# Kernel optimization log

Hardware: AMD Instinct MI355X
Metric: run time of the kernel (lower is better)

## Reference

```python
import jax, jax.numpy as jnp
import numpy as np

B, S, D = 4, 2048, 2048
H, KVH = 16, 8
HD = D // H          # 128
N_REP = H // KVH     # 2


def _rope(t, cos, sin):
    # t: [B,S,h,HD]; cos/sin: [S, HD//2]
    tr = t.reshape(*t.shape[:-1], HD // 2, 2)
    t0, t1 = tr[..., 0], tr[..., 1]
    c = cos[None, :, None, :]
    s = sin[None, :, None, :]
    o0 = t0 * c - t1 * s
    o1 = t0 * s + t1 * c
    return jnp.stack([o0, o1], axis=-1).reshape(t.shape)


def setup_inputs() -> dict:
    key = jax.random.key(0)
    ks = jax.random.split(key, 7)
    x = jax.random.normal(ks[0], (B, S, D), dtype=jnp.float32)
    wq = jax.random.normal(ks[1], (D, H * HD), dtype=jnp.float32) * 0.02
    wk = jax.random.normal(ks[2], (D, KVH * HD), dtype=jnp.float32) * 0.02
    wv = jax.random.normal(ks[3], (D, KVH * HD), dtype=jnp.float32) * 0.02
    wo = jax.random.normal(ks[4], (H * HD, D), dtype=jnp.float32) * 0.02
    # rotary angles as in precompute_pos_cis: theta=1e6-style base 10000
    freqs = 1.0 / (10000.0 ** (jnp.arange(0, HD, 2, dtype=jnp.float32) / HD))
    ang = jnp.outer(jnp.arange(S, dtype=jnp.float32), freqs)  # [S, HD//2]
    return {"x": x, "wq": wq, "wk": wk, "wv": wv, "wo": wo,
            "pos_cos": jnp.cos(ang), "pos_sin": jnp.sin(ang)}


def reference(x, wq, wk, wv, wo, pos_cos, pos_sin):
    q = (x @ wq).reshape(B, S, H, HD)
    k = (x @ wk).reshape(B, S, KVH, HD)
    v = (x @ wv).reshape(B, S, KVH, HD)
    q = _rope(q, pos_cos, pos_sin)
    k = _rope(k, pos_cos, pos_sin)
    # GQA repeat_kv: [B,S,KVH,HD] -> [B,S,H,HD]
    k = jnp.repeat(k, N_REP, axis=2)
    v = jnp.repeat(v, N_REP, axis=2)
    scale = 1.0 / jnp.sqrt(jnp.float32(HD))
    scores = jnp.einsum('bqhd,bkhd->bhqk', q, k) * scale
    causal = jnp.tril(jnp.ones((S, S), dtype=bool))
    scores = jnp.where(causal[None, None], scores, jnp.float32(-jnp.inf))
    attn = jax.nn.softmax(scores, axis=-1)
    out = jnp.einsum('bhqk,bkhd->bqhd', attn, v).reshape(B, S, H * HD)
    return out @ wo
```

## Files before the change

### kernel.cpp

```cpp
#include <hip/hip_runtime.h>
#include <stdint.h>

#define SEQ   2048
#define DIM   2048
#define NH    16
#define NKVH  8
#define HDIM  128
#define MTOT  8192
#define LOG2E 1.44269504088896340736f

typedef short bf16x8 __attribute__((ext_vector_type(8)));
typedef float f32x4  __attribute__((ext_vector_type(4)));
typedef unsigned short us4 __attribute__((ext_vector_type(4)));

#define MFMA(a, b, c) __builtin_amdgcn_mfma_f32_16x16x32_bf16((a), (b), (c), 0, 0, 0)

__device__ inline unsigned short f2bf(float f) {
    unsigned u = __builtin_bit_cast(unsigned, f);
    u = (u + 0x7FFFu + ((u >> 16) & 1u)) >> 16;
    return (unsigned short)u;
}

__device__ inline void stage16(const void* g, void* l) {
    __builtin_amdgcn_global_load_lds(
        (const __attribute__((address_space(1))) void*)g,
        (__attribute__((address_space(3))) void*)l,
        16, 0, 0);
}

__global__ void conv_x(const float* __restrict__ x, unsigned short* __restrict__ xb) {
    long i = ((long)blockIdx.x * 256 + threadIdx.x) * 4;
    float4 v = *(const float4*)(x + i);
    us4 o = { f2bf(v.x), f2bf(v.y), f2bf(v.z), f2bf(v.w) };
    *(us4*)(xb + i) = o;
}

__global__ void transpose_w(const float* __restrict__ in, unsigned short* __restrict__ out,
                            int N, int row_off) {
    __shared__ float t[32][33];
    int tx = threadIdx.x, ty = threadIdx.y;
    int n0 = blockIdx.x * 32, k0 = blockIdx.y * 32;
    for (int i = 0; i < 4; i++)
        t[ty + i * 8][tx] = in[(long)(k0 + ty + i * 8) * N + n0 + tx];
    __syncthreads();
    for (int i = 0; i < 4; i++)
        out[(long)(row_off + n0 + ty + i * 8) * 2048 + k0 + tx] = f2bf(t[tx][ty + i * 8]);
}

__global__ void transpose_v(const unsigned short* __restrict__ v, unsigned short* __restrict__ vt) {
    __shared__ unsigned short t[32][33];
    int tx = threadIdx.x, ty = threadIdx.y;
    int d0 = blockIdx.x * 32, s0 = blockIdx.y * 32, bk = blockIdx.z;
    const unsigned short* vin = v + (long)bk * SEQ * HDIM;
    unsigned short* vo = vt + (long)bk * HDIM * SEQ;
    for (int i = 0; i < 4; i++)
        t[ty + i * 8][tx] = vin[(long)(s0 + ty + i * 8) * HDIM + d0 + tx];
    __syncthreads();
    for (int i = 0; i < 4; i++)
        vo[(long)(d0 + ty + i * 8) * SEQ + s0 + tx] = t[tx][ty + i * 8];
}


#define STAGEH(p_, op_, h_, t_) do {                                              \
    unsigned short* d_ = sh + (p_) * 32768 + (op_) * 16384 + (h_) * 8192 + tid * 8; \
    const unsigned short* s_ = ((op_) ? bg : ag) + (long)((h_) * 128) * K + (t_) * 64; \
    stage16(s_, d_); stage16(s_ + 64 * K, d_ + 4096); } while (0)

#define BARRIER() asm volatile("s_barrier" ::: "memory")
#define WAITLGKM() asm volatile("s_waitcnt lgkmcnt(0)" ::: "memory")

__launch_bounds__(512, 2)
__global__ void qkv_gemm(const unsigned short* __restrict__ xb,
                         const unsigned short* __restrict__ wt,
                         const float* __restrict__ pcos, const float* __restrict__ psin,
                         unsigned short* __restrict__ qb, unsigned short* __restrict__ kbuf,
                         unsigned short* __restrict__ vbuf) {
    constexpr int K  = DIM;
    constexpr int NT = K / 64;
    __shared__ __align__(16) unsigned short sh[65536];
    const int tid = threadIdx.x;
    const int m0 = blockIdx.y * 256;
    const int n0 = blockIdx.x * 256;
    const int w = tid >> 6, lane = tid & 63, qq = lane >> 4, ln = lane & 15;
    const int wm = w >> 2, wn = w & 3;

    f32x4 acc[8][4] = {};

    const int rowq = tid >> 3;
    const int cswz = ((tid & 7) ^ (rowq & 7)) * 8;
    const unsigned short* ag = xb + (long)(m0 + rowq) * K + cswz;
    const unsigned short* bg = wt + (long)(n0 + rowq) * K + cswz;

    const int aoff = wm * 8192 + ln * 64;
    const int boff = 16384 + (wn >> 1) * 8192 + ((wn & 1) * 64 + ln) * 64;
    const int swz0 = ((0 + qq) ^ (ln & 7)) * 8;
    const int swz1 = ((4 + qq) ^ (ln & 7)) * 8;

    STAGEH(0, 1, 0, 0); STAGEH(0, 1, 1, 0); STAGEH(0, 0, 0, 0); STAGEH(0, 0, 1, 0);
    STAGEH(1, 1, 0, 1); STAGEH(1, 0, 0, 1); STAGEH(1, 0, 1, 1);

    #pragma unroll 1
    for (int t = 0; t < NT; t++) {
        const int p = t & 1, pn = p ^ 1;
        if (t >= NT - 1) asm volatile("s_waitcnt vmcnt(0)" ::: "memory");
        else             asm volatile("s_waitcnt vmcnt(6)" ::: "memory");
        BARRIER();

        const unsigned short* Ab = sh + p * 32768;
        bf16x8 af[8][2], bf_[4][2];

        #pragma unroll
        for (int fc = 0; fc < 4; fc++) {
            bf_[fc][0] = *(const bf16x8*)&Ab[boff + fc * 1024 + swz0];
            bf_[fc][1] = *(const bf16x8*)&Ab[boff + fc * 1024 + swz1];
        }
        #pragma unroll
        for (int fr = 0; fr < 4; fr++) {
            af[fr][0] = *(const bf16x8*)&Ab[aoff + fr * 1024 + swz0];
            af[fr][1] = *(const bf16x8*)&Ab[aoff + fr * 1024 + swz1];
        }
        if (t + 1 < NT) STAGEH(pn, 1, 1, t + 1);
        BARRIER();
        WAITLGKM();
        __builtin_amdgcn_s_setprio(1);
        #pragma unroll
        for (int fr = 0; fr < 4; fr++)
            #pragma unroll
            for (int fc = 0; fc < 2; fc++) {
                acc[fr][fc] = MFMA(bf_[fc][0], af[fr][0], acc[fr][fc]);
                acc[fr][fc] = MFMA(bf_[fc][1], af[fr][1], acc[fr][fc]);
            }
        __builtin_amdgcn_s_setprio(0);
        BARRIER();

        #pragma unroll
        for (int fr = 4; fr < 8; fr++) {
            af[fr][0] = *(const bf16x8*)&Ab[aoff + fr * 1024 + swz0];
            af[fr][1] = *(const bf16x8*)&Ab[aoff + fr * 1024 + swz1];
        }
        if (t + 2 < NT) STAGEH(p, 1, 0, t + 2);
        BARRIER();
        WAITLGKM();
        __builtin_amdgcn_s_setprio(1);
        #pragma unroll
        for (int fr = 0; fr < 4; fr++)
            #pragma unroll
            for (int fc = 2; fc < 4; fc++) {
                acc[fr][fc] = MFMA(bf_[fc][0], af[fr][0], acc[fr][fc]);
                acc[fr][fc] = MFMA(bf_[fc][1], af[fr][1], acc[fr][fc]);
            }
        __builtin_amdgcn_s_setprio(0);
        BARRIER();

        if (t + 2 < NT) STAGEH(p, 0, 0, t + 2);
        BARRIER();
        __builtin_amdgcn_s_setprio(1);
        #pragma unroll
        for (int fr = 4; fr < 8; fr++)
            #pragma unroll
            for (int fc = 0; fc < 2; fc++) {
                acc[fr][fc] = MFMA(bf_[fc][0], af[fr][0], acc[fr][fc]);
                acc[fr][fc] = MFMA(bf_[fc][1], af[fr][1], acc[fr][fc]);
            }
        __builtin_amdgcn_s_setprio(0);
        BARRIER();

        if (t + 2 < NT) STAGEH(p, 0, 1, t + 2);
        BARRIER();
        __builtin_amdgcn_s_setprio(1);
        #pragma unroll
        for (int fr = 4; fr < 8; fr++)
            #pragma unroll
            for (int fc = 2; fc < 4; fc++) {
                acc[fr][fc] = MFMA(bf_[fc][0], af[fr][0], acc[fr][fc]);
                acc[fr][fc] = MFMA(bf_[fc][1], af[fr][1], acc[fr][fc]);
            }
        __builtin_amdgcn_s_setprio(0);
        BARRIER();
    }

    const bool isv = (n0 >= 3072);
    for (int fr = 0; fr < 8; fr++) {
        int m = m0 + wm * 128 + fr * 16 + ln;
        int b_ = m >> 11, s = m & (SEQ - 1);
        const float* crow = pcos + s * 64;
        const float* srow = psin + s * 64;
        for (int fc = 0; fc < 4; fc++) {
            int n = n0 + wn * 64 + fc * 16 + qq * 4;
            int d = n & (HDIM - 1);
            f32x4 v = acc[fr][fc];
            float o0, o1, o2, o3;
            if (!isv) {
                int i = d >> 1;
                float2 cc = *(const float2*)(crow + i);
                float2 ss = *(const float2*)(srow + i);
                o0 = v[0] * cc.x - v[1] * ss.x;
                o1 = v[0] * ss.x + v[1] * cc.x;
                o2 = v[2] * cc.y - v[3] * ss.y;
                o3 = v[2] * ss.y + v[3] * cc.y;
            } else {
                o0 = v[0]; o1 = v[1]; o2 = v[2]; o3 = v[3];
            }
            us4 pu = { f2bf(o0), f2bf(o1), f2bf(o2), f2bf(o3) };
            if (n < 2048) {
                int hh = n >> 7;
                *(us4*)&qb[((long)(b_ * NH + hh) * SEQ + s) * HDIM + d] = pu;
            } else if (n < 3072) {
                int kvh = (n - 2048) >> 7;
                *(us4*)&kbuf[((long)(b_ * NKVH + kvh) * SEQ + s) * HDIM + d] = pu;
            } else {
                int kvh = (n - 3072) >> 7;
                *(us4*)&vbuf[((long)(b_ * NKVH + kvh) * SEQ + s) * HDIM + d] = pu;
            }
        }
    }
}

__launch_bounds__(256, 2)
__global__ void flash(const unsigned short* __restrict__ qb,
                      const unsigned short* __restrict__ kb,
                      const unsigned short* __restrict__ vtb,
                      unsigned short* __restrict__ aout) {
    __shared__ __align__(16) unsigned short KV[32768];
    const int tid = threadIdx.x;
    const int w = tid >> 6, lane = tid & 63, qq = lane >> 4, ln = lane & 15;
    unsigned short* Pseg = KV + w * 4096;

    int f = blockIdx.x + (blockIdx.y << 3) + (blockIdx.z << 7);
    int xcd = f & 7, j = f >> 3;
    int bkv = xcd + 8 * (j & 3);
    int b = bkv >> 3, kv = bkv & 7;
    int rem = j >> 2;
    int h = kv * 2 + (rem & 1);
    int qpair = rem >> 1;

    const unsigned short* qbase = qb + (long)(b * NH + h) * SEQ * HDIM;
    const unsigned short* kbase = kb + (long)(b * NKVH + kv) * SEQ * HDIM;
    const unsigned short* vbase = vtb + (long)(b * NKVH + kv) * HDIM * SEQ;
    const float SCL2 = 0.088388347648318447f * LOG2E;

    const int srow = tid >> 4;
    const int sswz = (tid & 15) ^ srow;

    for (int phase = 0; phase < 2; phase++) {
        const int qt = (phase == 0) ? qpair : 15 - qpair;
        const int q0 = qt * 128 + w * 32;

        bf16x8 qf[2][4];
        for (int nt = 0; nt < 2; nt++)
            for (int ks = 0; ks < 4; ks++)
                qf[nt][ks] = *(const bf16x8*)&qbase[(long)(q0 + nt * 16 + ln) * HDIM + ks * 32 + qq * 8];

        float m[2] = { -3e38f, -3e38f }, l[2] = { 0.f, 0.f };
        f32x4 oacc[8][2] = {};

        #pragma unroll 1
        for (int kt = 0; kt <= qt; kt++) {
            const int k0 = kt * 128;

            __syncthreads();
            char* kl = (char*)KV;
            #pragma unroll
            for (int r = 0; r < 8; r++) {
                int key = r * 16 + srow;
                stage16(kbase + (long)(k0 + key) * HDIM + sswz * 8, kl + r * 4096 + tid * 16);
            }
            #pragma unroll
            for (int r = 0; r < 8; r++) {
                int hd = r * 16 + srow;
                stage16(vbase + (long)hd * SEQ + k0 + sswz * 8, kl + 32768 + r * 4096 + tid * 16);
            }
            __syncthreads();

            f32x4 sacc[8][2] = {};
            #pragma unroll
            for (int mt = 0; mt < 8; mt++) {
                const unsigned short* kr = &KV[(mt * 16 + ln) * 128];
                bf16x8 kf0 = *(const bf16x8*)&kr[((0 + qq) ^ ln) * 8];
                bf16x8 kf1 = *(const bf16x8*)&kr[((4 + qq) ^ ln) * 8];
                bf16x8 kf2 = *(const bf16x8*)&kr[((8 + qq) ^ ln) * 8];
                bf16x8 kf3 = *(const bf16x8*)&kr[((12 + qq) ^ ln) * 8];
                sacc[mt][0] = MFMA(kf0, qf[0][0], sacc[mt][0]);
                sacc[mt][1] = MFMA(kf0, qf[1][0], sacc[mt][1]);
                sacc[mt][0] = MFMA(kf1, qf[0][1], sacc[mt][0]);
                sacc[mt][1] = MFMA(kf1, qf[1][1], sacc[mt][1]);
                sacc[mt][0] = MFMA(kf2, qf[0][2], sacc[mt][0]);
                sacc[mt][1] = MFMA(kf2, qf[1][2], sacc[mt][1]);
                sacc[mt][0] = MFMA(kf3, qf[0][3], sacc[mt][0]);
                sacc[mt][1] = MFMA(kf3, qf[1][3], sacc[mt][1]);
            }

            __syncthreads();

            const bool diag = (kt == qt);
            #pragma unroll
            for (int nt = 0; nt < 2; nt++) {
                const int q = q0 + nt * 16 + ln;
                float mx = m[nt];
                #pragma unroll
                for (int mt = 0; mt < 8; mt++)
                    #pragma unroll
                    for (int r = 0; r < 4; r++) {
                        float v = sacc[mt][nt][r];
                        if (diag && (k0 + mt * 16 + qq * 4 + r > q)) v = -3e38f;
                        sacc[mt][nt][r] = v;
                        mx = fmaxf(mx, v);
                    }
                mx = fmaxf(mx, __shfl_xor(mx, 16));
                mx = fmaxf(mx, __shfl_xor(mx, 32));
                float alpha = exp2f((m[nt] - mx) * SCL2);
                m[nt] = mx;
                float rs = 0.f;
                #pragma unroll
                for (int mt = 0; mt < 8; mt++) {
                    float p0 = exp2f((sacc[mt][nt][0] - mx) * SCL2);
                    float p1 = exp2f((sacc[mt][nt][1] - mx) * SCL2);
                    float p2 = exp2f((sacc[mt][nt][2] - mx) * SCL2);
                    float p3 = exp2f((sacc[mt][nt][3] - mx) * SCL2);
                    rs += (p0 + p1) + (p2 + p3);
                    us4 pu = { f2bf(p0), f2bf(p1), f2bf(p2), f2bf(p3) };
                    *(us4*)&Pseg[(nt * 16 + ln) * 128 + ((mt * 2 + (qq >> 1)) ^ ln) * 8 + (qq & 1) * 4] = pu;
                }
                rs += __shfl_xor(rs, 16);
                rs += __shfl_xor(rs, 32);
                l[nt] = l[nt] * alpha + rs;
                #pragma unroll
                for (int mt = 0; mt < 8; mt++)
                    #pragma unroll
                    for (int r = 0; r < 4; r++)
                        oacc[mt][nt][r] *= alpha;
            }

            bf16x8 pf[4][2];
            #pragma unroll
            for (int ks = 0; ks < 4; ks++)
                #pragma unroll
                for (int nt = 0; nt < 2; nt++)
                    pf[ks][nt] = *(const bf16x8*)&Pseg[(nt * 16 + ln) * 128 + ((ks * 4 + qq) ^ ln) * 8];
            #pragma unroll
            for (int mt = 0; mt < 8; mt++) {
                const unsigned short* vr = &KV[16384 + (mt * 16 + ln) * 128];
                bf16x8 vf0 = *(const bf16x8*)&vr[((0 + qq) ^ ln) * 8];
                bf16x8 vf1 = *(const bf16x8*)&vr[((4 + qq) ^ ln) * 8];
                bf16x8 vf2 = *(const bf16x8*)&vr[((8 + qq) ^ ln) * 8];
                bf16x8 vf3 = *(const bf16x8*)&vr[((12 + qq) ^ ln) * 8];
                oacc[mt][0] = MFMA(vf0, pf[0][0], oacc[mt][0]);
                oacc[mt][1] = MFMA(vf0, pf[0][1], oacc[mt][1]);
                oacc[mt][0] = MFMA(vf1, pf[1][0], oacc[mt][0]);
                oacc[mt][1] = MFMA(vf1, pf[1][1], oacc[mt][1]);
                oacc[mt][0] = MFMA(vf2, pf[2][0], oacc[mt][0]);
                oacc[mt][1] = MFMA(vf2, pf[2][1], oacc[mt][1]);
                oacc[mt][0] = MFMA(vf3, pf[3][0], oacc[mt][0]);
                oacc[mt][1] = MFMA(vf3, pf[3][1], oacc[mt][1]);
            }
        }

        #pragma unroll
        for (int nt = 0; nt < 2; nt++) {
            const int q = q0 + nt * 16 + ln;
            float inv = 1.f / l[nt];
            unsigned short* ao = aout + ((long)b * SEQ + q) * DIM + h * HDIM;
            #pragma unroll
            for (int mt = 0; mt < 8; mt++) {
                us4 o = { f2bf(oacc[mt][nt][0] * inv), f2bf(oacc[mt][nt][1] * inv),
                          f2bf(oacc[mt][nt][2] * inv), f2bf(oacc[mt][nt][3] * inv) };
                *(us4*)&ao[mt * 16 + qq * 4] = o;
            }
        }
    }
}

__launch_bounds__(512, 2)
__global__ void out_gemm(const unsigned short* __restrict__ ab,
                         const unsigned short* __restrict__ wt,
                         float* __restrict__ out) {
    constexpr int K  = DIM;
    constexpr int NT = K / 64;
    __shared__ __align__(16) unsigned short sh[65536];
    const int tid = threadIdx.x;
    const int m0 = blockIdx.y * 256;
    const int n0 = blockIdx.x * 256;
    const int w = tid >> 6, lane = tid & 63, qq = lane >> 4, ln = lane & 15;
    const int wm = w >> 2, wn = w & 3;

    f32x4 acc[8][4] = {};

    const int rowq = tid >> 3;
    const int cswz = ((tid & 7) ^ (rowq & 7)) * 8;
    const unsigned short* ag = ab + (long)(m0 + rowq) * K + cswz;
    const unsigned short* bg = wt + (long)(n0 + rowq) * K + cswz;

    const int aoff = wm * 8192 + ln * 64;
    const int boff = 16384 + (wn >> 1) * 8192 + ((wn & 1) * 64 + ln) * 64;
    const int swz0 = ((0 + qq) ^ (ln & 7)) * 8;
    const int swz1 = ((4 + qq) ^ (ln & 7)) * 8;

    STAGEH(0, 1, 0, 0); STAGEH(0, 1, 1, 0); STAGEH(0, 0, 0, 0); STAGEH(0, 0, 1, 0);
    STAGEH(1, 1, 0, 1); STAGEH(1, 0, 0, 1); STAGEH(1, 0, 1, 1);

    #pragma unroll 1
    for (int t = 0; t < NT; t++) {
        const int p = t & 1, pn = p ^ 1;
        if (t >= NT - 1) asm volatile("s_waitcnt vmcnt(0)" ::: "memory");
        else             asm volatile("s_waitcnt vmcnt(6)" ::: "memory");
        BARRIER();

        const unsigned short* Ab = sh + p * 32768;
        bf16x8 af[8][2], bf_[4][2];

        #pragma unroll
        for (int fc = 0; fc < 4; fc++) {
            bf_[fc][0] = *(const bf16x8*)&Ab[boff + fc * 1024 + swz0];
            bf_[fc][1] = *(const bf16x8*)&Ab[boff + fc * 1024 + swz1];
        }
        #pragma unroll
        for (int fr = 0; fr < 4; fr++) {
            af[fr][0] = *(const bf16x8*)&Ab[aoff + fr * 1024 + swz0];
            af[fr][1] = *(const bf16x8*)&Ab[aoff + fr * 1024 + swz1];
        }
        if (t + 1 < NT) STAGEH(pn, 1, 1, t + 1);
        BARRIER();
        WAITLGKM();
        __builtin_amdgcn_s_setprio(1);
        #pragma unroll
        for (int fr = 0; fr < 4; fr++)
            #pragma unroll
            for (int fc = 0; fc < 2; fc++) {
                acc[fr][fc] = MFMA(af[fr][0], bf_[fc][0], acc[fr][fc]);
                acc[fr][fc] = MFMA(af[fr][1], bf_[fc][1], acc[fr][fc]);
            }
        __builtin_amdgcn_s_setprio(0);
        BARRIER();

        #pragma unroll
        for (int fr = 4; fr < 8; fr++) {
            af[fr][0] = *(const bf16x8*)&Ab[aoff + fr * 1024 + swz0];
            af[fr][1] = *(const bf16x8*)&Ab[aoff + fr * 1024 + swz1];
        }
        if (t + 2 < NT) STAGEH(p, 1, 0, t + 2);
        BARRIER();
        WAITLGKM();
        __builtin_amdgcn_s_setprio(1);
        #pragma unroll
        for (int fr = 0; fr < 4; fr++)
            #pragma unroll
            for (int fc = 2; fc < 4; fc++) {
                acc[fr][fc] = MFMA(af[fr][0], bf_[fc][0], acc[fr][fc]);
                acc[fr][fc] = MFMA(af[fr][1], bf_[fc][1], acc[fr][fc]);
            }
        __builtin_amdgcn_s_setprio(0);
        BARRIER();

        if (t + 2 < NT) STAGEH(p, 0, 0, t + 2);
        BARRIER();
        __builtin_amdgcn_s_setprio(1);
        #pragma unroll
        for (int fr = 4; fr < 8; fr++)
            #pragma unroll
            for (int fc = 0; fc < 2; fc++) {
                acc[fr][fc] = MFMA(af[fr][0], bf_[fc][0], acc[fr][fc]);
                acc[fr][fc] = MFMA(af[fr][1], bf_[fc][1], acc[fr][fc]);
            }
        __builtin_amdgcn_s_setprio(0);
        BARRIER();

        if (t + 2 < NT) STAGEH(p, 0, 1, t + 2);
        BARRIER();
        __builtin_amdgcn_s_setprio(1);
        #pragma unroll
        for (int fr = 4; fr < 8; fr++)
            #pragma unroll
            for (int fc = 2; fc < 4; fc++) {
                acc[fr][fc] = MFMA(af[fr][0], bf_[fc][0], acc[fr][fc]);
                acc[fr][fc] = MFMA(af[fr][1], bf_[fc][1], acc[fr][fc]);
            }
        __builtin_amdgcn_s_setprio(0);
        BARRIER();
    }

    for (int fr = 0; fr < 8; fr++)
        for (int fc = 0; fc < 4; fc++) {
            int n = n0 + wn * 64 + fc * 16 + ln;
            for (int r = 0; r < 4; r++) {
                int m = m0 + wm * 128 + fr * 16 + qq * 4 + r;
                out[(long)m * DIM + n] = acc[fr][fc][r];
            }
        }
}

extern "C" void kernel_launch(void* const* d_in, const int* in_sizes, int n_in,
                              void* d_out, int out_size, void* d_ws, size_t ws_size,
                              hipStream_t stream) {
    const float* x    = (const float*)d_in[0];
    const float* wq   = (const float*)d_in[1];
    const float* wk   = (const float*)d_in[2];
    const float* wv   = (const float*)d_in[3];
    const float* wo   = (const float*)d_in[4];
    const float* pcos = (const float*)d_in[5];
    const float* psin = (const float*)d_in[6];
    float* out = (float*)d_out;

    char* ws = (char*)d_ws;
    unsigned short* xb    = (unsigned short*)(ws);
    unsigned short* wqkvt = (unsigned short*)(ws + 33554432L);
    unsigned short* wot   = (unsigned short*)(ws + 50331648L);
    unsigned short* qbuf  = (unsigned short*)(ws + 58720256L);
    unsigned short* kbuf  = (unsigned short*)(ws + 92274688L);
    unsigned short* vbuf  = (unsigned short*)(ws + 109051904L);
    unsigned short* vtb   = (unsigned short*)(ws + 125829120L);
    unsigned short* aout  = (unsigned short*)(ws + 142606336L);

    conv_x<<<16384, 256, 0, stream>>>(x, xb);
    transpose_w<<<dim3(64, 64), dim3(32, 8), 0, stream>>>(wq, wqkvt, 2048, 0);
    transpose_w<<<dim3(32, 64), dim3(32, 8), 0, stream>>>(wk, wqkvt, 1024, 2048);
    transpose_w<<<dim3(32, 64), dim3(32, 8), 0, stream>>>(wv, wqkvt, 1024, 3072);
    transpose_w<<<dim3(64, 64), dim3(32, 8), 0, stream>>>(wo, wot, 2048, 0);

    qkv_gemm<<<dim3(16, 32), 512, 0, stream>>>(xb, wqkvt, pcos, psin, qbuf, kbuf, vbuf);
    transpose_v<<<dim3(4, 64, 32), dim3(32, 8), 0, stream>>>(vbuf, vtb);
    flash<<<dim3(8, 16, 4), 256, 0, stream>>>(qbuf, kbuf, vtb, aout);
    out_gemm<<<dim3(8, 32), 512, 0, stream>>>(aout, wot, out);
}
```

Measured before the change: 512.1 us.

## Replace pipelined 256x256 QKV GEMM with simple 128x128 tile; raise MFMA priority in flash

The QKV projection GEMM drops its double-buffered, barrier-interleaved 256x256 tile schedule for a plain single-buffered 128x128 tile loop with 256 threads. The grid grows fourfold. Separately, the flash attention kernel wraps its QK and PV MFMA loops in s_setprio to favour matrix issue. The simpler GEMM loses overlap between global loads and compute and reuses less data per tile, so more memory traffic is likely. The extra blocks may help occupancy.

Result: slower. 544.7 us (+6.4%).

```diff
diff --git a/kernel.cpp b/kernel.cpp
--- a/kernel.cpp
+++ b/kernel.cpp
@@ -60,135 +60,64 @@
         vo[(long)(d0 + ty + i * 8) * SEQ + s0 + tx] = t[tx][ty + i * 8];
 }
 
-
-#define STAGEH(p_, op_, h_, t_) do {                                              \
-    unsigned short* d_ = sh + (p_) * 32768 + (op_) * 16384 + (h_) * 8192 + tid * 8; \
-    const unsigned short* s_ = ((op_) ? bg : ag) + (long)((h_) * 128) * K + (t_) * 64; \
-    stage16(s_, d_); stage16(s_ + 64 * K, d_ + 4096); } while (0)
-
-#define BARRIER() asm volatile("s_barrier" ::: "memory")
-#define WAITLGKM() asm volatile("s_waitcnt lgkmcnt(0)" ::: "memory")
-
-__launch_bounds__(512, 2)
+__launch_bounds__(256, 2)
 __global__ void qkv_gemm(const unsigned short* __restrict__ xb,
                          const unsigned short* __restrict__ wt,
                          const float* __restrict__ pcos, const float* __restrict__ psin,
                          unsigned short* __restrict__ qb, unsigned short* __restrict__ kbuf,
                          unsigned short* __restrict__ vbuf) {
-    constexpr int K  = DIM;
-    constexpr int NT = K / 64;
-    __shared__ __align__(16) unsigned short sh[65536];
+    constexpr int K = DIM;
+    __shared__ __align__(16) unsigned short As[128 * 64];
+    __shared__ __align__(16) unsigned short Bs[128 * 64];
     const int tid = threadIdx.x;
-    const int m0 = blockIdx.y * 256;
-    const int n0 = blockIdx.x * 256;
+    const int m0 = blockIdx.y * 128;
+    const int n0 = blockIdx.x * 128;
     const int w = tid >> 6, lane = tid & 63, qq = lane >> 4, ln = lane & 15;
-    const int wm = w >> 2, wn = w & 3;
-
-    f32x4 acc[8][4] = {};
-
-    const int rowq = tid >> 3;
-    const int cswz = ((tid & 7) ^ (rowq & 7)) * 8;
-    const unsigned short* ag = xb + (long)(m0 + rowq) * K + cswz;
-    const unsigned short* bg = wt + (long)(n0 + rowq) * K + cswz;
-
-    const int aoff = wm * 8192 + ln * 64;
-    const int boff = 16384 + (wn >> 1) * 8192 + ((wn & 1) * 64 + ln) * 64;
-    const int swz0 = ((0 + qq) ^ (ln & 7)) * 8;
-    const int swz1 = ((4 + qq) ^ (ln & 7)) * 8;
-
-    STAGEH(0, 1, 0, 0); STAGEH(0, 1, 1, 0); STAGEH(0, 0, 0, 0); STAGEH(0, 0, 1, 0);
-    STAGEH(1, 1, 0, 1); STAGEH(1, 0, 0, 1); STAGEH(1, 0, 1, 1);
-
-    #pragma unroll 1
-    for (int t = 0; t < NT; t++) {
-        const int p = t & 1, pn = p ^ 1;
-        if (t >= NT - 1) asm volatile("s_waitcnt vmcnt(0)" ::: "memory");
-        else             asm volatile("s_waitcnt vmcnt(6)" ::: "memory");
-        BARRIER();
-
-        const unsigned short* Ab = sh + p * 32768;
-        bf16x8 af[8][2], bf_[4][2];
-
-        #pragma unroll
-        for (int fc = 0; fc < 4; fc++) {
-            bf_[fc][0] = *(const bf16x8*)&Ab[boff + fc * 1024 + swz0];
-            bf_[fc][1] = *(const bf16x8*)&Ab[boff + fc * 1024 + swz1];
-        }
-        #pragma unroll
-        for (int fr = 0; fr < 4; fr++) {
-            af[fr][0] = *(const bf16x8*)&Ab[aoff + fr * 1024 + swz0];
-            af[fr][1] = *(const bf16x8*)&Ab[aoff + fr * 1024 + swz1];
-        }
-        if (t + 1 < NT) STAGEH(pn, 1, 1, t + 1);
-        BARRIER();
-        WAITLGKM();
-        __builtin_amdgcn_s_setprio(1);
-        #pragma unroll
-        for (int fr = 0; fr < 4; fr++)
-            #pragma unroll
-            for (int fc = 0; fc < 2; fc++) {
-                acc[fr][fc] = MFMA(bf_[fc][0], af[fr][0], acc[fr][fc]);
-                acc[fr][fc] = MFMA(bf_[fc][1], af[fr][1], acc[fr][fc]);
-            }
-        __builtin_amdgcn_s_setprio(0);
-        BARRIER();
-
-        #pragma unroll
-        for (int fr = 4; fr < 8; fr++) {
-            af[fr][0] = *(const bf16x8*)&Ab[aoff + fr * 1024 + swz0];
-            af[fr][1] = *(const bf16x8*)&Ab[aoff + fr * 1024 + swz1];
-        }
-        if (t + 2 < NT) STAGEH(p, 1, 0, t + 2);
-        BARRIER();
-        WAITLGKM();
-        __builtin_amdgcn_s_setprio(1);
-        #pragma unroll
-        for (int fr = 0; fr < 4; fr++)
-            #pragma unroll
-            for (int fc = 2; fc < 4; fc++) {
-                acc[fr][fc] = MFMA(bf_[fc][0], af[fr][0], acc[fr][fc]);
-                acc[fr][fc] = MFMA(bf_[fc][1], af[fr][1], acc[fr][fc]);
-            }
-        __builtin_amdgcn_s_setprio(0);
-        BARRIER();
-
-        if (t + 2 < NT) STAGEH(p, 0, 0, t + 2);
-        BARRIER();
-        __builtin_amdgcn_s_setprio(1);
-        #pragma unroll
-        for (int fr = 4; fr < 8; fr++)
-            #pragma unroll
-            for (int fc = 0; fc < 2; fc++) {
-                acc[fr][fc] = MFMA(bf_[fc][0], af[fr][0], acc[fr][fc]);
-                acc[fr][fc] = MFMA(bf_[fc][1], af[fr][1], acc[fr][fc]);
-            }
-        __builtin_amdgcn_s_setprio(0);
-        BARRIER();
-
-        if (t + 2 < NT) STAGEH(p, 0, 1, t + 2);
-        BARRIER();
-        __builtin_amdgcn_s_setprio(1);
-        #pragma unroll
-        for (int fr = 4; fr < 8; fr++)
-            #pragma unroll
-            for (int fc = 2; fc < 4; fc++) {
-                acc[fr][fc] = MFMA(bf_[fc][0], af[fr][0], acc[fr][fc]);
-                acc[fr][fc] = MFMA(bf_[fc][1], af[fr][1], acc[fr][fc]);
-            }
-        __builtin_amdgcn_s_setprio(0);
-        BARRIER();
+    const int wm = w >> 1, wn = w & 1;
+
+    f32x4 acc[4][4] = {};
+
+    const int arow = tid >> 3;
+    const int aswz = ((tid & 7) ^ (arow & 7)) * 8;
+    const unsigned short* ag = xb + (long)(m0 + arow) * K + aswz;
+    const unsigned short* bg = wt + (long)(n0 + arow) * K + aswz;
+    unsigned short* al = As + tid * 8;
+    unsigned short* bl = Bs + tid * 8;
+
+    for (int kk = 0; kk < K; kk += 64) {
+        __syncthreads();
+        stage16(ag + kk,          al);
+        stage16(ag + kk + 32 * K, al + 2048);
+        stage16(ag + kk + 64 * K, al + 4096);
+        stage16(ag + kk + 96 * K, al + 6144);
+        stage16(bg + kk,          bl);
+        stage16(bg + kk + 32 * K, bl + 2048);
+        stage16(bg + kk + 64 * K, bl + 4096);
+        stage16(bg + kk + 96 * K, bl + 6144);
+        __syncthreads();
+        bf16x8 a[2][4], b[2][4];
+        for (int ks = 0; ks < 2; ks++) {
+            for (int mt = 0; mt < 4; mt++)
+                a[ks][mt] = *(const bf16x8*)&As[(wm * 64 + mt * 16 + ln) * 64 + (((ks * 4 + qq) ^ (ln & 7)) * 8)];
+            for (int nt = 0; nt < 4; nt++)
+                b[ks][nt] = *(const bf16x8*)&Bs[(wn * 64 + nt * 16 + ln) * 64 + (((ks * 4 + qq) ^ (ln & 7)) * 8)];
+        }
+        for (int ks = 0; ks < 2; ks++)
+            for (int mt = 0; mt < 4; mt++)
+                for (int nt = 0; nt < 4; nt++)
+                    acc[mt][nt] = MFMA(b[ks][nt], a[ks][mt], acc[mt][nt]);
     }
 
     const bool isv = (n0 >= 3072);
-    for (int fr = 0; fr < 8; fr++) {
-        int m = m0 + wm * 128 + fr * 16 + ln;
+    for (int mt = 0; mt < 4; mt++) {
+        int m = m0 + wm * 64 + mt * 16 + ln;
         int b_ = m >> 11, s = m & (SEQ - 1);
         const float* crow = pcos + s * 64;
         const float* srow = psin + s * 64;
-        for (int fc = 0; fc < 4; fc++) {
-            int n = n0 + wn * 64 + fc * 16 + qq * 4;
+        for (int nt = 0; nt < 4; nt++) {
+            int n = n0 + wn * 64 + nt * 16 + qq * 4;
             int d = n & (HDIM - 1);
-            f32x4 v = acc[fr][fc];
+            f32x4 v = acc[mt][nt];
             float o0, o1, o2, o3;
             if (!isv) {
                 int i = d >> 1;
@@ -273,6 +202,7 @@
             __syncthreads();
 
             f32x4 sacc[8][2] = {};
+            __builtin_amdgcn_s_setprio(1);
             #pragma unroll
             for (int mt = 0; mt < 8; mt++) {
                 const unsigned short* kr = &KV[(mt * 16 + ln) * 128];
@@ -289,6 +219,7 @@
                 sacc[mt][0] = MFMA(kf3, qf[0][3], sacc[mt][0]);
                 sacc[mt][1] = MFMA(kf3, qf[1][3], sacc[mt][1]);
             }
+            __builtin_amdgcn_s_setprio(0);
 
             __syncthreads();
 
@@ -337,6 +268,7 @@
                 #pragma unroll
                 for (int nt = 0; nt < 2; nt++)
                     pf[ks][nt] = *(const bf16x8*)&Pseg[(nt * 16 + ln) * 128 + ((ks * 4 + qq) ^ ln) * 8];
+            __builtin_amdgcn_s_setprio(1);
             #pragma unroll
             for (int mt = 0; mt < 8; mt++) {
                 const unsigned short* vr = &KV[16384 + (mt * 16 + ln) * 128];
@@ -353,6 +285,7 @@
                 oacc[mt][0] = MFMA(vf3, pf[3][0], oacc[mt][0]);
                 oacc[mt][1] = MFMA(vf3, pf[3][1], oacc[mt][1]);
             }
+            __builtin_amdgcn_s_setprio(0);
         }
 
         #pragma unroll
@@ -369,6 +302,15 @@
         }
     }
 }
+
+
+#define STAGEH(p_, op_, h_, t_) do {                                              \
+    unsigned short* d_ = sh + (p_) * 32768 + (op_) * 16384 + (h_) * 8192 + tid * 8; \
+    const unsigned short* s_ = ((op_) ? bg : ag) + (long)((h_) * 128) * K + (t_) * 64; \
+    stage16(s_, d_); stage16(s_ + 64 * K, d_ + 4096); } while (0)
+
+#define BARRIER() asm volatile("s_barrier" ::: "memory")
+#define WAITLGKM() asm volatile("s_waitcnt lgkmcnt(0)" ::: "memory")
 
 __launch_bounds__(512, 2)
 __global__ void out_gemm(const unsigned short* __restrict__ ab,
@@ -516,7 +458,7 @@
     transpose_w<<<dim3(32, 64), dim3(32, 8), 0, stream>>>(wv, wqkvt, 1024, 3072);
     transpose_w<<<dim3(64, 64), dim3(32, 8), 0, stream>>>(wo, wot, 2048, 0);
 
-    qkv_gemm<<<dim3(16, 32), 512, 0, stream>>>(xb, wqkvt, pcos, psin, qbuf, kbuf, vbuf);
+    qkv_gemm<<<dim3(32, 64), 256, 0, stream>>>(xb, wqkvt, pcos, psin, qbuf, kbuf, vbuf);
     transpose_v<<<dim3(4, 64, 32), dim3(32, 8), 0, stream>>>(vbuf, vtb);
     flash<<<dim3(8, 16, 4), 256, 0, stream>>>(qbuf, kbuf, vtb, aout);
     out_gemm<<<dim3(8, 32), 512, 0, stream>>>(aout, wot, out);
```

## Simplify QKV GEMM pipeline, split attention waits, add lazy softmax rescaling

Applied to the files above, without the earlier changes.

The QKV GEMM drops its fine-grained half-tile staging, which had many barriers and setprio calls, and now issues one whole-tile prefetch per iteration with a single wait and barrier, interleaving LDS fragment loads with MFMAs. The attention kernel replaces __syncthreads with explicit vmcnt/lgkmcnt waits so the V tile load can overlap QK^T and softmax. Softmax now rescales the running max and output accumulators only when some lane's new max exceeds the old one by a threshold, which skips most alpha multiplies. The costs are less overlap between LDS stage writes and compute in the GEMM, and a threshold-based rescale that lets exponent values grow before renormalising.

After: 498.6 us. -2.6%, faster.

```diff
diff --git a/kernel.cpp b/kernel.cpp
--- a/kernel.cpp
+++ b/kernel.cpp
@@ -60,14 +60,19 @@
         vo[(long)(d0 + ty + i * 8) * SEQ + s0 + tx] = t[tx][ty + i * 8];
 }
 
-
-#define STAGEH(p_, op_, h_, t_) do {                                              \
-    unsigned short* d_ = sh + (p_) * 32768 + (op_) * 16384 + (h_) * 8192 + tid * 8; \
-    const unsigned short* s_ = ((op_) ? bg : ag) + (long)((h_) * 128) * K + (t_) * 64; \
-    stage16(s_, d_); stage16(s_ + 64 * K, d_ + 4096); } while (0)
-
-#define BARRIER() asm volatile("s_barrier" ::: "memory")
-#define WAITLGKM() asm volatile("s_waitcnt lgkmcnt(0)" ::: "memory")
+#define STAGET(p_, t_) do {                                                 \
+    unsigned short* da_ = sh + (p_) * 32768 + tid * 8;                      \
+    const unsigned short* sa_ = ag + (t_) * 64;                             \
+    const unsigned short* sb_ = bg + (t_) * 64;                             \
+    stage16(sa_,           da_);                                            \
+    stage16(sa_ + 64 * K,  da_ + 4096);                                     \
+    stage16(sa_ + 128 * K, da_ + 8192);                                     \
+    stage16(sa_ + 192 * K, da_ + 12288);                                    \
+    stage16(sb_,           da_ + 16384);                                    \
+    stage16(sb_ + 64 * K,  da_ + 20480);                                    \
+    stage16(sb_ + 128 * K, da_ + 24576);                                    \
+    stage16(sb_ + 192 * K, da_ + 28672);                                    \
+} while (0)
 
 __launch_bounds__(512, 2)
 __global__ void qkv_gemm(const unsigned short* __restrict__ xb,
@@ -96,18 +101,20 @@
     const int swz0 = ((0 + qq) ^ (ln & 7)) * 8;
     const int swz1 = ((4 + qq) ^ (ln & 7)) * 8;
 
-    STAGEH(0, 1, 0, 0); STAGEH(0, 1, 1, 0); STAGEH(0, 0, 0, 0); STAGEH(0, 0, 1, 0);
-    STAGEH(1, 1, 0, 1); STAGEH(1, 0, 0, 1); STAGEH(1, 0, 1, 1);
+    STAGET(0, 0);
+    STAGET(1, 1);
 
     #pragma unroll 1
     for (int t = 0; t < NT; t++) {
-        const int p = t & 1, pn = p ^ 1;
-        if (t >= NT - 1) asm volatile("s_waitcnt vmcnt(0)" ::: "memory");
-        else             asm volatile("s_waitcnt vmcnt(6)" ::: "memory");
-        BARRIER();
+        const int p = t & 1;
+        if (t == 0) asm volatile("s_waitcnt vmcnt(8)" ::: "memory");
+        else        asm volatile("s_waitcnt vmcnt(0)" ::: "memory");
+        asm volatile("s_barrier" ::: "memory");
+
+        if (t >= 1 && t + 1 < NT) STAGET(p ^ 1, t + 1);
 
         const unsigned short* Ab = sh + p * 32768;
-        bf16x8 af[8][2], bf_[4][2];
+        bf16x8 bf_[4][2], af[8][2];
 
         #pragma unroll
         for (int fc = 0; fc < 4; fc++) {
@@ -115,68 +122,53 @@
             bf_[fc][1] = *(const bf16x8*)&Ab[boff + fc * 1024 + swz1];
         }
         #pragma unroll
-        for (int fr = 0; fr < 4; fr++) {
+        for (int fr = 0; fr < 2; fr++) {
             af[fr][0] = *(const bf16x8*)&Ab[aoff + fr * 1024 + swz0];
             af[fr][1] = *(const bf16x8*)&Ab[aoff + fr * 1024 + swz1];
         }
-        if (t + 1 < NT) STAGEH(pn, 1, 1, t + 1);
-        BARRIER();
-        WAITLGKM();
-        __builtin_amdgcn_s_setprio(1);
-        #pragma unroll
-        for (int fr = 0; fr < 4; fr++)
-            #pragma unroll
-            for (int fc = 0; fc < 2; fc++) {
+        #pragma unroll
+        for (int fr = 2; fr < 4; fr++) {
+            af[fr][0] = *(const bf16x8*)&Ab[aoff + fr * 1024 + swz0];
+            af[fr][1] = *(const bf16x8*)&Ab[aoff + fr * 1024 + swz1];
+        }
+        #pragma unroll
+        for (int fr = 0; fr < 2; fr++)
+            #pragma unroll
+            for (int fc = 0; fc < 4; fc++) {
                 acc[fr][fc] = MFMA(bf_[fc][0], af[fr][0], acc[fr][fc]);
                 acc[fr][fc] = MFMA(bf_[fc][1], af[fr][1], acc[fr][fc]);
             }
-        __builtin_amdgcn_s_setprio(0);
-        BARRIER();
-
-        #pragma unroll
-        for (int fr = 4; fr < 8; fr++) {
+        #pragma unroll
+        for (int fr = 4; fr < 6; fr++) {
             af[fr][0] = *(const bf16x8*)&Ab[aoff + fr * 1024 + swz0];
             af[fr][1] = *(const bf16x8*)&Ab[aoff + fr * 1024 + swz1];
         }
-        if (t + 2 < NT) STAGEH(p, 1, 0, t + 2);
-        BARRIER();
-        WAITLGKM();
-        __builtin_amdgcn_s_setprio(1);
-        #pragma unroll
-        for (int fr = 0; fr < 4; fr++)
-            #pragma unroll
-            for (int fc = 2; fc < 4; fc++) {
+        #pragma unroll
+        for (int fr = 2; fr < 4; fr++)
+            #pragma unroll
+            for (int fc = 0; fc < 4; fc++) {
                 acc[fr][fc] = MFMA(bf_[fc][0], af[fr][0], acc[fr][fc]);
                 acc[fr][fc] = MFMA(bf_[fc][1], af[fr][1], acc[fr][fc]);
             }
-        __builtin_amdgcn_s_setprio(0);
-        BARRIER();
-
-        if (t + 2 < NT) STAGEH(p, 0, 0, t + 2);
-        BARRIER();
-        __builtin_amdgcn_s_setprio(1);
-        #pragma unroll
-        for (int fr = 4; fr < 8; fr++)
-            #pragma unroll
-            for (int fc = 0; fc < 2; fc++) {
+        #pragma unroll
+        for (int fr = 6; fr < 8; fr++) {
+            af[fr][0] = *(const bf16x8*)&Ab[aoff + fr * 1024 + swz0];
+            af[fr][1] = *(const bf16x8*)&Ab[aoff + fr * 1024 + swz1];
+        }
+        #pragma unroll
+        for (int fr = 4; fr < 6; fr++)
+            #pragma unroll
+            for (int fc = 0; fc < 4; fc++) {
                 acc[fr][fc] = MFMA(bf_[fc][0], af[fr][0], acc[fr][fc]);
                 acc[fr][fc] = MFMA(bf_[fc][1], af[fr][1], acc[fr][fc]);
             }
-        __builtin_amdgcn_s_setprio(0);
-        BARRIER();
-
-        if (t + 2 < NT) STAGEH(p, 0, 1, t + 2);
-        BARRIER();
-        __builtin_amdgcn_s_setprio(1);
-        #pragma unroll
-        for (int fr = 4; fr < 8; fr++)
-            #pragma unroll
-            for (int fc = 2; fc < 4; fc++) {
+        #pragma unroll
+        for (int fr = 6; fr < 8; fr++)
+            #pragma unroll
+            for (int fc = 0; fc < 4; fc++) {
                 acc[fr][fc] = MFMA(bf_[fc][0], af[fr][0], acc[fr][fc]);
                 acc[fr][fc] = MFMA(bf_[fc][1], af[fr][1], acc[fr][fc]);
             }
-        __builtin_amdgcn_s_setprio(0);
-        BARRIER();
     }
 
     const bool isv = (n0 >= 3072);
@@ -270,7 +262,8 @@
                 int hd = r * 16 + srow;
                 stage16(vbase + (long)hd * SEQ + k0 + sswz * 8, kl + 32768 + r * 4096 + tid * 16);
             }
-            __syncthreads();
+            asm volatile("s_waitcnt vmcnt(8)" ::: "memory");
+            asm volatile("s_barrier" ::: "memory");
 
             f32x4 sacc[8][2] = {};
             #pragma unroll
@@ -290,13 +283,14 @@
                 sacc[mt][1] = MFMA(kf3, qf[1][3], sacc[mt][1]);
             }
 
-            __syncthreads();
+            asm volatile("s_waitcnt lgkmcnt(0)" ::: "memory");
+            asm volatile("s_barrier" ::: "memory");
 
             const bool diag = (kt == qt);
             #pragma unroll
             for (int nt = 0; nt < 2; nt++) {
                 const int q = q0 + nt * 16 + ln;
-                float mx = m[nt];
+                float mx = -3e38f;
                 #pragma unroll
                 for (int mt = 0; mt < 8; mt++)
                     #pragma unroll
@@ -308,28 +302,35 @@
                     }
                 mx = fmaxf(mx, __shfl_xor(mx, 16));
                 mx = fmaxf(mx, __shfl_xor(mx, 32));
-                float alpha = exp2f((m[nt] - mx) * SCL2);
-                m[nt] = mx;
+                if (!__all(mx <= m[nt] + 62.7f)) {
+                    float newm = fmaxf(m[nt], mx);
+                    float alpha = exp2f((m[nt] - newm) * SCL2);
+                    l[nt] *= alpha;
+                    #pragma unroll
+                    for (int mt = 0; mt < 8; mt++)
+                        #pragma unroll
+                        for (int r = 0; r < 4; r++)
+                            oacc[mt][nt][r] *= alpha;
+                    m[nt] = newm;
+                }
                 float rs = 0.f;
                 #pragma unroll
                 for (int mt = 0; mt < 8; mt++) {
-                    float p0 = exp2f((sacc[mt][nt][0] - mx) * SCL2);
-                    float p1 = exp2f((sacc[mt][nt][1] - mx) * SCL2);
-                    float p2 = exp2f((sacc[mt][nt][2] - mx) * SCL2);
-                    float p3 = exp2f((sacc[mt][nt][3] - mx) * SCL2);
+                    float p0 = exp2f((sacc[mt][nt][0] - m[nt]) * SCL2);
+                    float p1 = exp2f((sacc[mt][nt][1] - m[nt]) * SCL2);
+                    float p2 = exp2f((sacc[mt][nt][2] - m[nt]) * SCL2);
+                    float p3 = exp2f((sacc[mt][nt][3] - m[nt]) * SCL2);
                     rs += (p0 + p1) + (p2 + p3);
                     us4 pu = { f2bf(p0), f2bf(p1), f2bf(p2), f2bf(p3) };
                     *(us4*)&Pseg[(nt * 16 + ln) * 128 + ((mt * 2 + (qq >> 1)) ^ ln) * 8 + (qq & 1) * 4] = pu;
                 }
                 rs += __shfl_xor(rs, 16);
                 rs += __shfl_xor(rs, 32);
-                l[nt] = l[nt] * alpha + rs;
-                #pragma unroll
-                for (int mt = 0; mt < 8; mt++)
-                    #pragma unroll
-                    for (int r = 0; r < 4; r++)
-                        oacc[mt][nt][r] *= alpha;
-            }
+                l[nt] += rs;
+            }
+
+            asm volatile("s_waitcnt vmcnt(0)" ::: "memory");
+            asm volatile("s_barrier" ::: "memory");
 
             bf16x8 pf[4][2];
             #pragma unroll
@@ -370,6 +371,15 @@
     }
 }
 
+
+#define STAGEH(p_, op_, h_, t_) do {                                              \
+    unsigned short* d_ = sh + (p_) * 32768 + (op_) * 16384 + (h_) * 8192 + tid * 8; \
+    const unsigned short* s_ = ((op_) ? bg : ag) + (long)((h_) * 128) * K + (t_) * 64; \
+    stage16(s_, d_); stage16(s_ + 64 * K, d_ + 4096); } while (0)
+
+#define BARRIER() asm volatile("s_barrier" ::: "memory")
+#define WAITLGKM() asm volatile("s_waitcnt lgkmcnt(0)" ::: "memory")
+
 __launch_bounds__(512, 2)
 __global__ void out_gemm(const unsigned short* __restrict__ ab,
                          const unsigned short* __restrict__ wt,
```
